# Performance work log

Hardware: AMD Instinct MI355X
Metric: run time of the kernel (lower is better)

The kernel has to match this reference:

```python
import jax, jax.numpy as jnp
import numpy as np

C_IN, C_OUT, H = 8, 8, 16
N1D = 20                      # 1D quadrature points -> 400 mesh nodes in 2D
B = 16
DECAY = (N1D / 4.0) ** 4      # set_quad: decay_param = (N/4)**4


def _quad_mesh():
    # Gauss-Legendre nodes/weights on [-1,1], tensor-product in 2D (get_quad_mesh)
    x, w = np.polynomial.legendre.leggauss(N1D)
    X, Y = np.meshgrid(x, x, indexing='xy')
    WX, WY = np.meshgrid(w, w, indexing='xy')
    nodes = np.dstack([X, Y]).reshape(-1, 2).astype(np.float32)
    weights = (WX * WY).reshape(-1).astype(np.float32)
    return nodes, weights


def setup_inputs() -> dict:
    key = jax.random.key(0)
    k1, k2, k3, k4 = jax.random.split(key, 4)
    nodes, w = _quad_mesh()
    K = C_IN * C_OUT
    return {
        'features': jax.random.normal(k1, (B, C_IN, N1D * N1D), jnp.float32),
        # 64 tiny MLPs (Linear no bias + Sin), spec (2,16,16,1), stacked on axis 0
        'W1': jax.random.normal(k2, (K, H, 2), jnp.float32) / np.sqrt(2.0),
        'W2': jax.random.normal(k3, (K, H, H), jnp.float32) / np.sqrt(float(H)),
        'W3': jax.random.normal(k4, (K, 1, H), jnp.float32) / np.sqrt(float(H)),
        'output_locs': jnp.asarray(nodes),   # (M,2) same tensor-product mesh
        'mesh_nodes': jnp.asarray(nodes),    # (N,2)
        'mesh_weights': jnp.asarray(w),      # (N,) product of 1D weights
    }


def _kernel(W1, W2, W3, output_locs, mesh_nodes):
    # pairwise eval points z = y_m - x_n, shape (M, N, 2)
    z = output_locs[:, None, :] - mesh_nodes[None, :, :]
    M, N, _ = z.shape
    zf = z.reshape(M * N, 2)
    # batched tiny MLPs: Linear -> Sin -> Linear -> Sin -> Linear (no bias)
    h = jnp.sin(jnp.einsum('khd,pd->kph', W1, zf))
    h = jnp.sin(jnp.einsum('koh,kph->kpo', W2, h))
    kv = jnp.einsum('koh,kph->kpo', W3, h)[..., 0]          # (K, M*N)
    # bump function enforcing compact support: exp(1 - 1/(1 - c*||z||^4))
    bump_arg = jnp.sum(zf * zf, axis=-1) ** 2               # ||z||^4
    inside = bump_arg < 1.0 / DECAY
    safe = jnp.where(inside, 1.0 - DECAY * bump_arg, 1.0)
    bump = jnp.where(inside, jnp.exp(1.0 - 1.0 / safe), 0.0)
    kv = kv * bump[None, :]
    return kv.reshape(C_OUT, C_IN, M, N)


def reference(features, W1, W2, W3, output_locs, mesh_nodes, mesh_weights):
    Kmat = _kernel(W1, W2, W3, output_locs, mesh_nodes)     # (Co,Ci,M,N)
    # quadrature-weighted conv sum: out[b,o,m] = sum_{i,n} K[o,i,m,n] w[n] f[b,i,n]
    return jnp.einsum('oimn,n,bin->bom', Kmat, mesh_weights, features)
```

## Files before the change

kernel.cpp:

```cpp
#include <hip/hip_runtime.h>
#include <math.h>

#define CIN   8
#define COUT  8
#define HH    16
#define NN    400
#define MM    400
#define BB    16

#define THREADS 512
#define PMAX    32
#define NGRP    16
#define MPG     25
#define PPG     16
#define NPAGES  (NGRP*PPG)
#define MAXNM   12

#define WS_FT   0
#define WS_L    (NN*CIN*BB)
#define WS_CNT  (WS_L + MM*PMAX*4)
#define WS_PM0  (WS_CNT + MM)
#define WS_PNM  (WS_PM0 + NPAGES)

__device__ __forceinline__ bool bump_inside(float zx, float zy, float& a) {
    float s = __fadd_rn(__fmul_rn(zx, zx), __fmul_rn(zy, zy));
    a = __fmul_rn(s, s);
    return a < (1.0f / 625.0f);
}

__global__ __launch_bounds__(THREADS) void prep_kernel(
    const float* __restrict__ f,
    const float* __restrict__ locs,
    const float* __restrict__ nodes,
    const float* __restrict__ wq,
    float* __restrict__ ws)
{
    const int blk = blockIdx.x;
    const int t   = threadIdx.x;

    if (blk < 100) {
        int idx = blk * 512 + t;
        int b = idx / 3200;
        int r = idx - b * 3200;
        int i = r / 400;
        int n = r - i * 400;
        ws[WS_FT + n*128 + b*8 + i] = f[idx];
    } else if (blk < 150) {
        const int lane = t & 63;
        const int w    = t >> 6;
        const int m    = (blk - 100) * 8 + w;
        const float2 y = ((const float2*)locs)[m];
        const float2* nd = (const float2*)nodes;
        float4* lst = (float4*)(ws + WS_L);
        int cnt = 0;
        for (int n0 = 0; n0 < NN; n0 += 64) {
            int n = n0 + lane;
            bool in = false;
            float zx = 0.f, zy = 0.f, bwv = 0.f;
            if (n < NN) {
                float2 x = nd[n];
                zx = y.x - x.x; zy = y.y - x.y;
                float a;
                if (bump_inside(zx, zy, a)) {
                    in = true;
                    bwv = __expf(1.0f - 1.0f/(1.0f - 625.0f*a)) * wq[n];
                }
            }
            unsigned long long msk = __ballot(in);
            int idx = cnt + __popcll(msk & ((1ull << lane) - 1ull));
            if (in && idx < PMAX)
                lst[m*PMAX + idx] = make_float4(zx, zy, bwv, __int_as_float(n));
            cnt += __popcll(msk);
        }
        if (lane >= cnt && lane < PMAX)
            lst[m*PMAX + lane] = make_float4(0.f, 0.f, 0.f, __int_as_float(0));
    } else {
        __shared__ float dx2[400], dy2[400];
        __shared__ int   scnt[400];
        if (t < 400) {
            int i = t / 20, j = t % 20;
            float zx = locs[2*i]          - nodes[2*j];
            float zy = locs[2*(i*20) + 1] - nodes[2*(j*20) + 1];
            dx2[t] = __fmul_rn(zx, zx);
            dy2[t] = __fmul_rn(zy, zy);
        }
        __syncthreads();
        if (t < 400) {
            int mx = t % 20, my = t / 20;
            int c = 0;
            for (int ny = 0; ny < 20; ++ny) {
                float dyv = dy2[my*20 + ny];
                for (int nx = 0; nx < 20; ++nx) {
                    float s = __fadd_rn(dx2[mx*20 + nx], dyv);
                    float a = __fmul_rn(s, s);
                    c += (a < (1.0f / 625.0f)) ? 1 : 0;
                }
            }
            c = min(c, PMAX);
            scnt[t] = c;
            ((int*)ws)[WS_CNT + t] = c;
        }
        __syncthreads();
        if (t < NGRP) {
            int* pm0 = (int*)ws + WS_PM0;
            int* pnm = (int*)ws + WS_PNM;
            const int m0g = t * MPG, mend = m0g + MPG;
            int p = t * PPG;
            int cur0 = m0g, used = 0;
            for (int m = m0g; m < mend; ++m) {
                int c = scnt[m];
                if (used + c > 64) {
                    pm0[p] = cur0; pnm[p] = m - cur0; ++p;
                    cur0 = m; used = 0;
                }
                used += c;
            }
            pm0[p] = cur0; pnm[p] = mend - cur0; ++p;
            for (; p < (t + 1) * PPG; ++p) { pm0[p] = 0; pnm[p] = 0; }
        }
    }
}

__global__ __launch_bounds__(THREADS) void quadconv_kernel(
    const float* __restrict__ W1,
    const float* __restrict__ W2,
    const float* __restrict__ W3,
    const float* __restrict__ ws,
    float* __restrict__ out)
{
    __shared__ float s_w2[8*256];
    __shared__ float s_w1[8*32];
    __shared__ float s_w3[8*16];
    __shared__ float s_kv[8*64];
    __shared__ float s_pp[64*17];
    __shared__ int   s_pn[64];
    __shared__ int   s_off[MAXNM + 1];
    __shared__ int   s_m0;

    const int t    = threadIdx.x;
    const int lane = t & 63;
    const int w    = __builtin_amdgcn_readfirstlane(t >> 6);
    const int p    = blockIdx.x >> 3;
    const int kg   = blockIdx.x & 7;

    const int nm = ((const int*)ws)[WS_PNM + p];
    if (nm == 0) return;
    const int m0 = ((const int*)ws)[WS_PM0 + p];

    {
        const float4* W2v = (const float4*)(W2 + kg * 8 * 256);
        ((float4*)s_w2)[t] = W2v[t];
        if (t < 64) ((float4*)s_w1)[t] = ((const float4*)(W1 + kg * 8 * 32))[t];
        if (t < 32) ((float4*)s_w3)[t] = ((const float4*)(W3 + kg * 8 * 16))[t];
    }
    if (w == 0) {
        int c = (lane < nm) ? ((const int*)ws)[WS_CNT + m0 + lane] : 0;
        #pragma unroll
        for (int d = 1; d < 16; d <<= 1) {
            int u = __shfl_up(c, d);
            if (lane >= d) c += u;
        }
        if (lane < nm) s_off[lane + 1] = c;
        if (lane == 0) { s_off[0] = 0; s_m0 = m0; }
    }
    __syncthreads();

    int seg = 0;
    #pragma unroll
    for (int sgi = 1; sgi < MAXNM; ++sgi)
        seg += (sgi < nm && lane >= s_off[sgi]) ? 1 : 0;
    const int used = s_off[nm];
    float4 sv = make_float4(0.f, 0.f, 0.f, 0.f);
    int n_id = 0;
    if (lane < used) {
        const int m  = m0 + seg;
        const int jj = lane - s_off[seg];
        sv = ((const float4*)(ws + WS_L))[m * PMAX + jj];
        n_id = __float_as_int(sv.w);
    }
    if (t < 64) s_pn[t] = n_id;

    {
        const float* __restrict__ w1 = s_w1 + w * 32;
        const float* __restrict__ w2 = s_w2 + w * 256;
        const float* __restrict__ w3 = s_w3 + w * 16;
        const float zx = sv.x, zy = sv.y, bw = sv.z;

        float h1[HH];
        #pragma unroll
        for (int j = 0; j < HH; ++j)
            h1[j] = __sinf(w1[2*j] * zx + w1[2*j + 1] * zy);

        float kv = 0.f;
        #pragma unroll
        for (int oo = 0; oo < HH; ++oo) {
            float d = 0.f;
            #pragma unroll
            for (int j = 0; j < HH; ++j)
                d += w2[oo*HH + j] * h1[j];
            kv += w3[oo] * __sinf(d);
        }
        s_kv[w*64 + lane] = kv * bw;
    }
    __syncthreads();

    {
        const int j  = t >> 3;
        const int b0 = t & 7;
        const int n  = s_pn[j];
        const float* __restrict__ fb = ws + WS_FT + n*128;
        float4 A0 = *(const float4*)(fb + b0*8);
        float4 A1 = *(const float4*)(fb + b0*8 + 4);
        float4 B0 = *(const float4*)(fb + (b0+8)*8);
        float4 B1 = *(const float4*)(fb + (b0+8)*8 + 4);
        float k0 = s_kv[0*64 + j], k1 = s_kv[1*64 + j];
        float k2 = s_kv[2*64 + j], k3 = s_kv[3*64 + j];
        float k4 = s_kv[4*64 + j], k5 = s_kv[5*64 + j];
        float k6 = s_kv[6*64 + j], k7 = s_kv[7*64 + j];
        float pA = k0*A0.x + k1*A0.y + k2*A0.z + k3*A0.w
                 + k4*A1.x + k5*A1.y + k6*A1.z + k7*A1.w;
        float pB = k0*B0.x + k1*B0.y + k2*B0.z + k3*B0.w
                 + k4*B1.x + k5*B1.y + k6*B1.z + k7*B1.w;
        s_pp[j*17 + b0]     = pA;
        s_pp[j*17 + b0 + 8] = pB;
    }
    __syncthreads();

    if (t < nm * 16) {
        const int b    = t & 15;
        const int sidx = t >> 4;
        const int lo   = s_off[sidx];
        const int hi   = s_off[sidx + 1];
        float acc = 0.f;
        for (int j = lo; j < hi; ++j)
            acc += s_pp[j*17 + b];
        out[b * (COUT*MM) + kg * MM + (s_m0 + sidx)] = acc;
    }
}

extern "C" void kernel_launch(void* const* d_in, const int* in_sizes, int n_in,
                              void* d_out, int out_size, void* d_ws, size_t ws_size,
                              hipStream_t stream) {
    const float* f     = (const float*)d_in[0];
    const float* W1    = (const float*)d_in[1];
    const float* W2    = (const float*)d_in[2];
    const float* W3    = (const float*)d_in[3];
    const float* locs  = (const float*)d_in[4];
    const float* nodes = (const float*)d_in[5];
    const float* wq    = (const float*)d_in[6];
    float* out = (float*)d_out;
    float* ws  = (float*)d_ws;

    prep_kernel<<<dim3(151), dim3(THREADS), 0, stream>>>(f, locs, nodes, wq, ws);
    quadconv_kernel<<<dim3(NPAGES * 8), dim3(THREADS), 0, stream>>>(
        W1, W2, W3, ws, out);
}
```

Before: 24.24 us.

## Process two pair-pages per block to amortize weight staging and add ILP

Each block now handles two consecutive pages of (m,n) pairs instead of one, which halves the quadconv grid. The per-block shared-memory load of the W1/W2/W3 weight slices is shared across both pages. The MLP evaluation interleaves the two pages so each W2 row, now read as float4, feeds two dot products, adding instruction-level parallelism. The trade-off is higher register and shared-memory use per block and fewer blocks to spread across CUs, and a block whose second page is empty still computes that lane's MLP.

```diff
diff --git a/kernel.cpp b/kernel.cpp
--- a/kernel.cpp
+++ b/kernel.cpp
@@ -131,21 +131,22 @@
     __shared__ float s_w2[8*256];
     __shared__ float s_w1[8*32];
     __shared__ float s_w3[8*16];
-    __shared__ float s_kv[8*64];
-    __shared__ float s_pp[64*17];
-    __shared__ int   s_pn[64];
-    __shared__ int   s_off[MAXNM + 1];
-    __shared__ int   s_m0;
+    __shared__ float s_kvT[2][64*10];
+    __shared__ float s_pp[2][64*17];
+    __shared__ int   s_pn[2][64];
+    __shared__ int   s_off[2][MAXNM + 1];
+    __shared__ int   s_m0[2];
 
     const int t    = threadIdx.x;
     const int lane = t & 63;
     const int w    = __builtin_amdgcn_readfirstlane(t >> 6);
-    const int p    = blockIdx.x >> 3;
+    const int pp   = blockIdx.x >> 3;
     const int kg   = blockIdx.x & 7;
-
-    const int nm = ((const int*)ws)[WS_PNM + p];
-    if (nm == 0) return;
-    const int m0 = ((const int*)ws)[WS_PM0 + p];
+    const int pA   = pp * 2;
+
+    const int nmA = ((const int*)ws)[WS_PNM + pA];
+    const int nmB = ((const int*)ws)[WS_PNM + pA + 1];
+    if (nmA == 0) return;
 
     {
         const float4* W2v = (const float4*)(W2 + kg * 8 * 256);
@@ -153,88 +154,120 @@
         if (t < 64) ((float4*)s_w1)[t] = ((const float4*)(W1 + kg * 8 * 32))[t];
         if (t < 32) ((float4*)s_w3)[t] = ((const float4*)(W3 + kg * 8 * 16))[t];
     }
-    if (w == 0) {
+    if (w < 2) {
+        const int nm = (w == 0) ? nmA : nmB;
+        const int m0 = ((const int*)ws)[WS_PM0 + pA + w];
         int c = (lane < nm) ? ((const int*)ws)[WS_CNT + m0 + lane] : 0;
         #pragma unroll
         for (int d = 1; d < 16; d <<= 1) {
             int u = __shfl_up(c, d);
             if (lane >= d) c += u;
         }
-        if (lane < nm) s_off[lane + 1] = c;
-        if (lane == 0) { s_off[0] = 0; s_m0 = m0; }
+        if (lane < nm) s_off[w][lane + 1] = c;
+        if (lane == 0) { s_off[w][0] = 0; s_m0[w] = m0; }
     }
     __syncthreads();
 
-    int seg = 0;
+    float4 sv[2];
+    int    n_id[2];
     #pragma unroll
-    for (int sgi = 1; sgi < MAXNM; ++sgi)
-        seg += (sgi < nm && lane >= s_off[sgi]) ? 1 : 0;
-    const int used = s_off[nm];
-    float4 sv = make_float4(0.f, 0.f, 0.f, 0.f);
-    int n_id = 0;
-    if (lane < used) {
-        const int m  = m0 + seg;
-        const int jj = lane - s_off[seg];
-        sv = ((const float4*)(ws + WS_L))[m * PMAX + jj];
-        n_id = __float_as_int(sv.w);
-    }
-    if (t < 64) s_pn[t] = n_id;
+    for (int pg = 0; pg < 2; ++pg) {
+        const int nm = (pg == 0) ? nmA : nmB;
+        int seg = 0;
+        #pragma unroll
+        for (int sgi = 1; sgi < MAXNM; ++sgi)
+            seg += (sgi < nm && lane >= s_off[pg][sgi]) ? 1 : 0;
+        const int used = s_off[pg][nm];
+        float4 v = make_float4(0.f, 0.f, 0.f, 0.f);
+        int nid = 0;
+        if (lane < used) {
+            const int m  = s_m0[pg] + seg;
+            const int jj = lane - s_off[pg][seg];
+            v = ((const float4*)(ws + WS_L))[m * PMAX + jj];
+            nid = __float_as_int(v.w);
+        }
+        sv[pg] = v; n_id[pg] = nid;
+    }
+    if (w == 0) s_pn[0][lane] = n_id[0];
+    if (w == 1) s_pn[1][lane] = n_id[1];
 
     {
         const float* __restrict__ w1 = s_w1 + w * 32;
-        const float* __restrict__ w2 = s_w2 + w * 256;
-        const float* __restrict__ w3 = s_w3 + w * 16;
-        const float zx = sv.x, zy = sv.y, bw = sv.z;
-
-        float h1[HH];
-        #pragma unroll
-        for (int j = 0; j < HH; ++j)
-            h1[j] = __sinf(w1[2*j] * zx + w1[2*j + 1] * zy);
-
-        float kv = 0.f;
+        const float* __restrict__ w3p = s_w3 + w * 16;
+        float4 w3q[4];
+        #pragma unroll
+        for (int q = 0; q < 4; ++q) w3q[q] = ((const float4*)w3p)[q];
+        float w3r[16] = {w3q[0].x, w3q[0].y, w3q[0].z, w3q[0].w,
+                         w3q[1].x, w3q[1].y, w3q[1].z, w3q[1].w,
+                         w3q[2].x, w3q[2].y, w3q[2].z, w3q[2].w,
+                         w3q[3].x, w3q[3].y, w3q[3].z, w3q[3].w};
+
+        float h1A[HH], h1B[HH];
+        #pragma unroll
+        for (int j = 0; j < HH; ++j) {
+            float wa = w1[2*j], wb = w1[2*j + 1];
+            h1A[j] = __sinf(wa * sv[0].x + wb * sv[0].y);
+            h1B[j] = __sinf(wa * sv[1].x + wb * sv[1].y);
+        }
+        float kvA = 0.f, kvB = 0.f;
+        const float4* __restrict__ w2v = (const float4*)(s_w2 + w * 256);
         #pragma unroll
         for (int oo = 0; oo < HH; ++oo) {
-            float d = 0.f;
-            #pragma unroll
-            for (int j = 0; j < HH; ++j)
-                d += w2[oo*HH + j] * h1[j];
-            kv += w3[oo] * __sinf(d);
-        }
-        s_kv[w*64 + lane] = kv * bw;
+            float4 r0 = w2v[oo*4+0], r1 = w2v[oo*4+1],
+                   r2 = w2v[oo*4+2], r3 = w2v[oo*4+3];
+            float dA = r0.x*h1A[0] + r0.y*h1A[1] + r0.z*h1A[2] + r0.w*h1A[3]
+                     + r1.x*h1A[4] + r1.y*h1A[5] + r1.z*h1A[6] + r1.w*h1A[7]
+                     + r2.x*h1A[8] + r2.y*h1A[9] + r2.z*h1A[10]+ r2.w*h1A[11]
+                     + r3.x*h1A[12]+ r3.y*h1A[13]+ r3.z*h1A[14]+ r3.w*h1A[15];
+            float dB = r0.x*h1B[0] + r0.y*h1B[1] + r0.z*h1B[2] + r0.w*h1B[3]
+                     + r1.x*h1B[4] + r1.y*h1B[5] + r1.z*h1B[6] + r1.w*h1B[7]
+                     + r2.x*h1B[8] + r2.y*h1B[9] + r2.z*h1B[10]+ r2.w*h1B[11]
+                     + r3.x*h1B[12]+ r3.y*h1B[13]+ r3.z*h1B[14]+ r3.w*h1B[15];
+            kvA += w3r[oo] * __sinf(dA);
+            kvB += w3r[oo] * __sinf(dB);
+        }
+        s_kvT[0][lane*10 + w] = kvA * sv[0].z;
+        s_kvT[1][lane*10 + w] = kvB * sv[1].z;
     }
     __syncthreads();
 
     {
         const int j  = t >> 3;
         const int b0 = t & 7;
-        const int n  = s_pn[j];
-        const float* __restrict__ fb = ws + WS_FT + n*128;
-        float4 A0 = *(const float4*)(fb + b0*8);
-        float4 A1 = *(const float4*)(fb + b0*8 + 4);
-        float4 B0 = *(const float4*)(fb + (b0+8)*8);
-        float4 B1 = *(const float4*)(fb + (b0+8)*8 + 4);
-        float k0 = s_kv[0*64 + j], k1 = s_kv[1*64 + j];
-        float k2 = s_kv[2*64 + j], k3 = s_kv[3*64 + j];
-        float k4 = s_kv[4*64 + j], k5 = s_kv[5*64 + j];
-        float k6 = s_kv[6*64 + j], k7 = s_kv[7*64 + j];
-        float pA = k0*A0.x + k1*A0.y + k2*A0.z + k3*A0.w
-                 + k4*A1.x + k5*A1.y + k6*A1.z + k7*A1.w;
-        float pB = k0*B0.x + k1*B0.y + k2*B0.z + k3*B0.w
-                 + k4*B1.x + k5*B1.y + k6*B1.z + k7*B1.w;
-        s_pp[j*17 + b0]     = pA;
-        s_pp[j*17 + b0 + 8] = pB;
+        #pragma unroll
+        for (int pg = 0; pg < 2; ++pg) {
+            const int n = s_pn[pg][j];
+            const float* __restrict__ fb = ws + WS_FT + n*128;
+            float4 A0 = *(const float4*)(fb + b0*8);
+            float4 A1 = *(const float4*)(fb + b0*8 + 4);
+            float4 B0 = *(const float4*)(fb + (b0+8)*8);
+            float4 B1 = *(const float4*)(fb + (b0+8)*8 + 4);
+            const float* kr = &s_kvT[pg][j*10];
+            float k0 = kr[0], k1 = kr[1], k2 = kr[2], k3 = kr[3];
+            float k4 = kr[4], k5 = kr[5], k6 = kr[6], k7 = kr[7];
+            float pAcc = k0*A0.x + k1*A0.y + k2*A0.z + k3*A0.w
+                       + k4*A1.x + k5*A1.y + k6*A1.z + k7*A1.w;
+            float pBcc = k0*B0.x + k1*B0.y + k2*B0.z + k3*B0.w
+                       + k4*B1.x + k5*B1.y + k6*B1.z + k7*B1.w;
+            s_pp[pg][j*17 + b0]     = pAcc;
+            s_pp[pg][j*17 + b0 + 8] = pBcc;
+        }
     }
     __syncthreads();
 
-    if (t < nm * 16) {
-        const int b    = t & 15;
-        const int sidx = t >> 4;
-        const int lo   = s_off[sidx];
-        const int hi   = s_off[sidx + 1];
-        float acc = 0.f;
-        for (int j = lo; j < hi; ++j)
-            acc += s_pp[j*17 + b];
-        out[b * (COUT*MM) + kg * MM + (s_m0 + sidx)] = acc;
+    #pragma unroll
+    for (int pg = 0; pg < 2; ++pg) {
+        const int nm = (pg == 0) ? nmA : nmB;
+        if (t < nm * 16) {
+            const int b    = t & 15;
+            const int sidx = t >> 4;
+            const int lo   = s_off[pg][sidx];
+            const int hi   = s_off[pg][sidx + 1];
+            float acc = 0.f;
+            for (int j = lo; j < hi; ++j)
+                acc += s_pp[pg][j*17 + b];
+            out[b * (COUT*MM) + kg * MM + (s_m0[pg] + sidx)] = acc;
+        }
     }
 }
 
@@ -252,6 +285,6 @@
     float* ws  = (float*)d_ws;
 
     prep_kernel<<<dim3(151), dim3(THREADS), 0, stream>>>(f, locs, nodes, wq, ws);
-    quadconv_kernel<<<dim3(NPAGES * 8), dim3(THREADS), 0, stream>>>(
+    quadconv_kernel<<<dim3((NPAGES/2) * 8), dim3(THREADS), 0, stream>>>(
         W1, W2, W3, ws, out);
 }
```

After: 28.99 us. 19.6% more time.
